# Performance work log

Hardware: AMD Instinct MI355X
Metric: run time of the kernel (lower is better)

The kernel has to match this reference:

```python
import jax, jax.numpy as jnp
import numpy as np

N_NODES = 100000


def sage_conv(x, src, dst, w_self, w_nei, b):
    # mean aggregation over incoming edges (src -> dst)
    agg = jax.ops.segment_sum(x[src], dst, num_segments=N_NODES)          # [N, d]
    deg = jax.ops.segment_sum(jnp.ones((src.shape[0], 1), x.dtype), dst,
                              num_segments=N_NODES)                        # [N, 1]
    mean = agg / jnp.maximum(deg, 1.0)
    return x @ w_self + mean @ w_nei + b


def setup_inputs() -> dict:
    key = jax.random.key(0)
    ks = jax.random.split(key, 12)
    d_in, d_hid, d_out = 64, 64, 64
    E = 1600000
    s = lambda d: 1.0 / np.sqrt(d)
    return {
        "x": jax.random.normal(ks[0], (N_NODES, d_in), jnp.float32),
        "edge_index": jax.random.randint(ks[1], (2, E), 0, N_NODES, jnp.int64),
        "w_self1": jax.random.normal(ks[2], (d_in, d_hid), jnp.float32) * s(d_in),
        "w_nei1": jax.random.normal(ks[3], (d_in, d_hid), jnp.float32) * s(d_in),
        "b1": jnp.zeros((d_hid,), jnp.float32),
        "w_self2": jax.random.normal(ks[4], (d_hid, d_hid), jnp.float32) * s(d_hid),
        "w_nei2": jax.random.normal(ks[5], (d_hid, d_hid), jnp.float32) * s(d_hid),
        "b2": jnp.zeros((d_hid,), jnp.float32),
        "w_self3": jax.random.normal(ks[6], (d_hid, d_out), jnp.float32) * s(d_hid),
        "w_nei3": jax.random.normal(ks[7], (d_hid, d_out), jnp.float32) * s(d_hid),
        "b3": jnp.zeros((d_out,), jnp.float32),
    }


def reference(x, edge_index, w_self1, w_nei1, b1, w_self2, w_nei2, b2,
              w_self3, w_nei3, b3):
    src, dst = edge_index[0], edge_index[1]
    h = jax.nn.relu(sage_conv(x, src, dst, w_self1, w_nei1, b1))
    h = jax.nn.relu(sage_conv(h, src, dst, w_self2, w_nei2, b2))
    h = sage_conv(h, src, dst, w_self3, w_nei3, b3)
    return h
```

## Files before the change

### kernel.cpp

```cpp
#include <hip/hip_runtime.h>
#include <hip/hip_bf16.h>

#define PB   512

typedef short bf16x8 __attribute__((ext_vector_type(8)));
typedef float f32x4  __attribute__((ext_vector_type(4)));

__device__ __forceinline__ unsigned short f2bf(float f) {
    unsigned u = __float_as_uint(f);
    u += 0x7FFFu + ((u >> 16) & 1u);
    return (unsigned short)(u >> 16);
}


__global__ __launch_bounds__(256) void part_hist(const int* __restrict__ dst,
                                                 int* __restrict__ counts,
                                                 int E, int NB) {
    __shared__ int h[512];
    const int tid = threadIdx.x;
    for (int i = tid; i < NB; i += 256) h[i] = 0;
    __syncthreads();
    const int per = (E + PB - 1) / PB;
    const int s = blockIdx.x * per;
    const int e = min(E, s + per);
    for (int i = s + tid; i < e; i += 256) atomicAdd(&h[dst[i] >> 8], 1);
    __syncthreads();
    for (int i = tid; i < NB; i += 256) counts[i * PB + blockIdx.x] = h[i];
}

__global__ __launch_bounds__(256) void scanA(const int* __restrict__ in,
                                             int* __restrict__ excl,
                                             int* __restrict__ bsums, int M) {
    __shared__ int tmp[256];
    const int tid = threadIdx.x;
    const int g = blockIdx.x * 256 + tid;
    int v = (g < M) ? in[g] : 0;
    tmp[tid] = v;
    __syncthreads();
    for (int off = 1; off < 256; off <<= 1) {
        int t = (tid >= off) ? tmp[tid - off] : 0;
        __syncthreads();
        tmp[tid] += t;
        __syncthreads();
    }
    if (g < M) excl[g] = tmp[tid] - v;
    if (tid == 255) bsums[blockIdx.x] = tmp[255];
}

__global__ __launch_bounds__(1024) void scanB(int* bsums, int nb) {
    __shared__ int tmp[1024];
    const int tid = threadIdx.x;
    int v = (tid < nb) ? bsums[tid] : 0;
    tmp[tid] = v;
    __syncthreads();
    for (int off = 1; off < 1024; off <<= 1) {
        int t = (tid >= off) ? tmp[tid - off] : 0;
        __syncthreads();
        tmp[tid] += t;
        __syncthreads();
    }
    if (tid < nb) bsums[tid] = tmp[tid] - v;
}

__global__ __launch_bounds__(256) void scanC(int* __restrict__ seg_base,
                                             const int* __restrict__ bsums,
                                             int* __restrict__ bucket_base,
                                             int M, int NB, int E) {
    const int g = blockIdx.x * 256 + threadIdx.x;
    if (g < M) {
        const int v = seg_base[g] + bsums[g >> 8];
        seg_base[g] = v;
        if ((g & (PB - 1)) == 0) bucket_base[g / PB] = v;
    }
    if (g == 0) bucket_base[NB] = E;
}

__global__ __launch_bounds__(256) void part_scatter(const int* __restrict__ src,
                                                    const int* __restrict__ dst,
                                                    const int* __restrict__ seg_base,
                                                    int* __restrict__ pairs,
                                                    int E, int NB) {
    __shared__ int cur[512];
    const int tid = threadIdx.x;
    for (int i = tid; i < NB; i += 256) cur[i] = seg_base[i * PB + blockIdx.x];
    __syncthreads();
    const int per = (E + PB - 1) / PB;
    const int s = blockIdx.x * per;
    const int e = min(E, s + per);
    for (int i = s + tid; i < e; i += 256) {
        const int d = dst[i];
        const int b = d >> 8;
        const int slot = atomicAdd(&cur[b], 1);
        pairs[slot] = src[i] | ((d & 255) << 20);
    }
}

__global__ __launch_bounds__(256) void csr_finalize(const int* __restrict__ pairs,
                                                    const int* __restrict__ bucket_base,
                                                    int* __restrict__ row_start,
                                                    int* __restrict__ col,
                                                    int N, int E) {
    __shared__ int h[256];
    __shared__ int tmp[256];
    __shared__ int cur[256];
    const int tid = threadIdx.x;
    const int b = blockIdx.x;
    const int node0 = b << 8;
    const int pbeg = bucket_base[b];
    const int pend = bucket_base[b + 1];
    h[tid] = 0;
    __syncthreads();
    for (int i = pbeg + tid; i < pend; i += 256)
        atomicAdd(&h[(pairs[i] >> 20) & 255], 1);
    __syncthreads();
    const int v = h[tid];
    tmp[tid] = v;
    __syncthreads();
    for (int off = 1; off < 256; off <<= 1) {
        int t = (tid >= off) ? tmp[tid - off] : 0;
        __syncthreads();
        tmp[tid] += t;
        __syncthreads();
    }
    const int excl = tmp[tid] - v;
    cur[tid] = pbeg + excl;
    if (node0 + tid < N) row_start[node0 + tid] = pbeg + excl;
    if (b == 0 && tid == 0) row_start[N] = E;
    __syncthreads();
    for (int i = pbeg + tid; i < pend; i += 256) {
        const int p = pairs[i];
        const int slot = atomicAdd(&cur[(p >> 20) & 255], 1);
        col[slot] = p & 0xFFFFF;
    }
}

__global__ __launch_bounds__(256) void to_bf16_kernel(const float* __restrict__ in,
                                                      unsigned short* __restrict__ out,
                                                      int n8) {
    const int g = blockIdx.x * 256 + threadIdx.x;
    if (g >= n8) return;
    const float4 v0 = *(const float4*)(in + (size_t)g * 8);
    const float4 v1 = *(const float4*)(in + (size_t)g * 8 + 4);
    uint4 o;
    o.x = (unsigned)f2bf(v0.x) | ((unsigned)f2bf(v0.y) << 16);
    o.y = (unsigned)f2bf(v0.z) | ((unsigned)f2bf(v0.w) << 16);
    o.z = (unsigned)f2bf(v1.x) | ((unsigned)f2bf(v1.y) << 16);
    o.w = (unsigned)f2bf(v1.z) | ((unsigned)f2bf(v1.w) << 16);
    *(uint4*)(out + (size_t)g * 8) = o;
}

__global__ __launch_bounds__(256) void pack_w_kernel(const float* __restrict__ Ws,
                                                     const float* __restrict__ Wn,
                                                     unsigned short* __restrict__ bswp) {
    const int i = blockIdx.x * 256 + threadIdx.x;
    if (i >= 8192) return;
    const int j = i & 7;
    const int L = (i >> 3) & 63;
    const int t = (i >> 9) & 3;
    const int s = i >> 11;
    const int k = s * 32 + ((L >> 4) << 3) + j;
    const int n = t * 16 + (L & 15);
    const float v = (k < 64) ? Ws[k * 64 + n] : Wn[(k - 64) * 64 + n];
    bswp[i] = f2bf(v);
}

#define ACC8(A, V)                                                    \
    A##0 += __uint_as_float((V).x << 16);                             \
    A##1 += __uint_as_float((V).x & 0xFFFF0000u);                     \
    A##2 += __uint_as_float((V).y << 16);                             \
    A##3 += __uint_as_float((V).y & 0xFFFF0000u);                     \
    A##4 += __uint_as_float((V).z << 16);                             \
    A##5 += __uint_as_float((V).z & 0xFFFF0000u);                     \
    A##6 += __uint_as_float((V).w << 16);                             \
    A##7 += __uint_as_float((V).w & 0xFFFF0000u);

__global__ __launch_bounds__(256) void gather_mean_kernel(
        const unsigned short* __restrict__ xb, const int* __restrict__ col,
        const int* __restrict__ row_start, unsigned short* __restrict__ meanb, int N) {
    const int tid = threadIdx.x;
    const int node = blockIdx.x * 32 + (tid >> 3);
    const int c8 = (tid & 7) * 8;
    if (node >= N) return;
    const int beg = row_start[node];
    const int end = row_start[node + 1];

    float a0 = 0.f, a1 = 0.f, a2 = 0.f, a3 = 0.f, a4 = 0.f, a5 = 0.f, a6 = 0.f, a7 = 0.f;
    float b0 = 0.f, b1 = 0.f, b2 = 0.f, b3 = 0.f, b4 = 0.f, b5 = 0.f, b6 = 0.f, b7 = 0.f;

    int i = beg;
    for (; i + 4 <= end; i += 4) {
        const int s0 = col[i + 0];
        const int s1 = col[i + 1];
        const int s2 = col[i + 2];
        const int s3 = col[i + 3];
        const uint4 v0 = *(const uint4*)(xb + (size_t)s0 * 64 + c8);
        const uint4 v1 = *(const uint4*)(xb + (size_t)s1 * 64 + c8);
        const uint4 v2 = *(const uint4*)(xb + (size_t)s2 * 64 + c8);
        const uint4 v3 = *(const uint4*)(xb + (size_t)s3 * 64 + c8);
        ACC8(a, v0)
        ACC8(b, v1)
        ACC8(a, v2)
        ACC8(b, v3)
    }
    for (; i < end; ++i) {
        const int s = col[i];
        const uint4 v = *(const uint4*)(xb + (size_t)s * 64 + c8);
        ACC8(a, v)
    }

    const float rd = 1.0f / fmaxf((float)(end - beg), 1.0f);
    const float m0 = (a0 + b0) * rd, m1 = (a1 + b1) * rd;
    const float m2 = (a2 + b2) * rd, m3 = (a3 + b3) * rd;
    const float m4 = (a4 + b4) * rd, m5 = (a5 + b5) * rd;
    const float m6 = (a6 + b6) * rd, m7 = (a7 + b7) * rd;
    uint4 o;
    o.x = (unsigned)f2bf(m0) | ((unsigned)f2bf(m1) << 16);
    o.y = (unsigned)f2bf(m2) | ((unsigned)f2bf(m3) << 16);
    o.z = (unsigned)f2bf(m4) | ((unsigned)f2bf(m5) << 16);
    o.w = (unsigned)f2bf(m6) | ((unsigned)f2bf(m7) << 16);
    *(uint4*)(meanb + (size_t)node * 64 + c8) = o;
}

__global__ __launch_bounds__(256) void mfma_update_kernel(
        const unsigned short* __restrict__ xb,
        const unsigned short* __restrict__ meanb,
        const unsigned short* __restrict__ bswp,
        const float* __restrict__ bias,
        float* __restrict__ outf,
        unsigned short* __restrict__ outb,
        int N, int do_relu) {
    const int tid  = threadIdx.x;
    const int lane = tid & 63;
    const int wave = tid >> 6;
    const int m    = lane & 15;
    const int quad = lane >> 4;
    const int node0 = blockIdx.x * 64 + wave * 16;

    int arow = node0 + m;
    if (arow >= N) arow = N - 1;
    const unsigned short* xr = xb    + (size_t)arow * 64 + quad * 8;
    const unsigned short* mr = meanb + (size_t)arow * 64 + quad * 8;

    f32x4 acc[4];
#pragma unroll
    for (int t = 0; t < 4; ++t) {
        const float b = bias[t * 16 + m];
        acc[t] = (f32x4){b, b, b, b};
    }

#pragma unroll
    for (int s = 0; s < 4; ++s) {
        bf16x8 a;
        if (s < 2) a = *(const bf16x8*)(xr + s * 32);
        else       a = *(const bf16x8*)(mr + (s - 2) * 32);
#pragma unroll
        for (int t = 0; t < 4; ++t) {
            const bf16x8 bf = *(const bf16x8*)(bswp + (((s * 4 + t) * 64 + lane) << 3));
            acc[t] = __builtin_amdgcn_mfma_f32_16x16x32_bf16(a, bf, acc[t], 0, 0, 0);
        }
    }

#pragma unroll
    for (int t = 0; t < 4; ++t) {
        const int colg = t * 16 + m;
#pragma unroll
        for (int r = 0; r < 4; ++r) {
            const int node = node0 + quad * 4 + r;
            if (node < N) {
                float v = acc[t][r];
                if (do_relu) v = fmaxf(v, 0.f);
                if (outf) outf[(size_t)node * 64 + colg] = v;
                if (outb) outb[(size_t)node * 64 + colg] = f2bf(v);
            }
        }
    }
}

extern "C" void kernel_launch(void* const* d_in, const int* in_sizes, int n_in,
                              void* d_out, int out_size, void* d_ws, size_t ws_size,
                              hipStream_t stream) {
    const float* x   = (const float*)d_in[0];
    const int*   ei  = (const int*)d_in[1];
    const float* ws1 = (const float*)d_in[2];
    const float* wn1 = (const float*)d_in[3];
    const float* b1  = (const float*)d_in[4];
    const float* ws2 = (const float*)d_in[5];
    const float* wn2 = (const float*)d_in[6];
    const float* b2  = (const float*)d_in[7];
    const float* ws3 = (const float*)d_in[8];
    const float* wn3 = (const float*)d_in[9];
    const float* b3  = (const float*)d_in[10];

    const int N = in_sizes[0] / 64;
    const int E = in_sizes[1] / 2;
    const int* src = ei;
    const int* dst = ei + E;
    const int NB = (N + 255) >> 8;
    const int M  = NB * PB;

    float* out = (float*)d_out;

    auto align256 = [](size_t v) { return (v + 255) / 256 * 256; };
    char* p = (char*)d_ws;
    int* counts      = (int*)p; p += align256((size_t)M * 4);
    int* seg_base    = (int*)p; p += align256((size_t)M * 4);
    int* bsums       = (int*)p; p += align256(1024 * 4);
    int* bucket_base = (int*)p; p += align256((size_t)(NB + 1) * 4);
    int* row_start   = (int*)p; p += align256((size_t)(N + 1) * 4);
    int* pairs       = (int*)p; p += align256((size_t)E * 4);
    int* col         = (int*)p; p += align256((size_t)E * 4);
    unsigned short* xb    = (unsigned short*)p; p += align256((size_t)N * 64 * 2);
    unsigned short* meanb = (unsigned short*)p; p += align256((size_t)N * 64 * 2);
    unsigned short* bw1   = (unsigned short*)p; p += align256(8192 * 2);
    unsigned short* bw2   = (unsigned short*)p; p += align256(8192 * 2);
    unsigned short* bw3   = (unsigned short*)p; p += align256(8192 * 2);

    const int scan_blocks = (M + 255) / 256;
    const int gm_blocks   = (N + 31) / 32;
    const int upd_blocks  = (N + 63) / 64;
    const int cvt_blocks  = (N * 64 / 8 + 255) / 256;

    part_hist   <<<PB, 256, 0, stream>>>(dst, counts, E, NB);
    scanA       <<<scan_blocks, 256, 0, stream>>>(counts, seg_base, bsums, M);
    scanB       <<<1, 1024, 0, stream>>>(bsums, scan_blocks);
    scanC       <<<scan_blocks, 256, 0, stream>>>(seg_base, bsums, bucket_base, M, NB, E);
    part_scatter<<<PB, 256, 0, stream>>>(src, dst, seg_base, pairs, E, NB);
    csr_finalize<<<NB, 256, 0, stream>>>(pairs, bucket_base, row_start, col, N, E);

    pack_w_kernel<<<32, 256, 0, stream>>>(ws1, wn1, bw1);
    pack_w_kernel<<<32, 256, 0, stream>>>(ws2, wn2, bw2);
    pack_w_kernel<<<32, 256, 0, stream>>>(ws3, wn3, bw3);
    to_bf16_kernel<<<cvt_blocks, 256, 0, stream>>>(x, xb, N * 64 / 8);

    gather_mean_kernel<<<gm_blocks, 256, 0, stream>>>(xb, col, row_start, meanb, N);
    mfma_update_kernel<<<upd_blocks, 256, 0, stream>>>(xb, meanb, bw1, b1, nullptr, xb, N, 1);
    gather_mean_kernel<<<gm_blocks, 256, 0, stream>>>(xb, col, row_start, meanb, N);
    mfma_update_kernel<<<upd_blocks, 256, 0, stream>>>(xb, meanb, bw2, b2, nullptr, xb, N, 1);
    gather_mean_kernel<<<gm_blocks, 256, 0, stream>>>(xb, col, row_start, meanb, N);
    mfma_update_kernel<<<upd_blocks, 256, 0, stream>>>(xb, meanb, bw3, b3, out, nullptr, N, 0);
}
```

Baseline: 276.4 us.

## Fuse neighbor mean gather with MFMA update per layer and batch weight packing

Merges the gather-mean and MFMA linear update into one kernel per layer. Each block computes the bf16 means for its 64 nodes into shared memory and then feeds them straight to the MFMA. This removes the global round trip of the mean buffer and three kernel launches. Ping-pong feature buffers replace the in-place update, since other blocks may still be gathering the old features. The three weight-pack launches are merged into one. The cost is that each block now spends longer in the irregular gather before its MFMA phase.

```diff
diff --git a/kernel.cpp b/kernel.cpp
--- a/kernel.cpp
+++ b/kernel.cpp
@@ -149,19 +149,25 @@
     *(uint4*)(out + (size_t)g * 8) = o;
 }
 
-__global__ __launch_bounds__(256) void pack_w_kernel(const float* __restrict__ Ws,
-                                                     const float* __restrict__ Wn,
-                                                     unsigned short* __restrict__ bswp) {
+__global__ __launch_bounds__(256) void pack_w3_kernel(
+        const float* __restrict__ Ws1, const float* __restrict__ Wn1,
+        const float* __restrict__ Ws2, const float* __restrict__ Wn2,
+        const float* __restrict__ Ws3, const float* __restrict__ Wn3,
+        unsigned short* __restrict__ bw) {
     const int i = blockIdx.x * 256 + threadIdx.x;
-    if (i >= 8192) return;
-    const int j = i & 7;
-    const int L = (i >> 3) & 63;
-    const int t = (i >> 9) & 3;
-    const int s = i >> 11;
+    if (i >= 3 * 8192) return;
+    const int w = i >> 13;
+    const int r = i & 8191;
+    const float* Ws = (w == 0) ? Ws1 : (w == 1) ? Ws2 : Ws3;
+    const float* Wn = (w == 0) ? Wn1 : (w == 1) ? Wn2 : Wn3;
+    const int j = r & 7;
+    const int L = (r >> 3) & 63;
+    const int t = (r >> 9) & 3;
+    const int s = r >> 11;
     const int k = s * 32 + ((L >> 4) << 3) + j;
     const int n = t * 16 + (L & 15);
     const float v = (k < 64) ? Ws[k * 64 + n] : Wn[(k - 64) * 64 + n];
-    bswp[i] = f2bf(v);
+    bw[i] = f2bf(v);
 }
 
 #define ACC8(A, V)                                                    \
@@ -174,72 +180,72 @@
     A##6 += __uint_as_float((V).w << 16);                             \
     A##7 += __uint_as_float((V).w & 0xFFFF0000u);
 
-__global__ __launch_bounds__(256) void gather_mean_kernel(
-        const unsigned short* __restrict__ xb, const int* __restrict__ col,
-        const int* __restrict__ row_start, unsigned short* __restrict__ meanb, int N) {
-    const int tid = threadIdx.x;
-    const int node = blockIdx.x * 32 + (tid >> 3);
-    const int c8 = (tid & 7) * 8;
-    if (node >= N) return;
-    const int beg = row_start[node];
-    const int end = row_start[node + 1];
-
-    float a0 = 0.f, a1 = 0.f, a2 = 0.f, a3 = 0.f, a4 = 0.f, a5 = 0.f, a6 = 0.f, a7 = 0.f;
-    float b0 = 0.f, b1 = 0.f, b2 = 0.f, b3 = 0.f, b4 = 0.f, b5 = 0.f, b6 = 0.f, b7 = 0.f;
-
-    int i = beg;
-    for (; i + 4 <= end; i += 4) {
-        const int s0 = col[i + 0];
-        const int s1 = col[i + 1];
-        const int s2 = col[i + 2];
-        const int s3 = col[i + 3];
-        const uint4 v0 = *(const uint4*)(xb + (size_t)s0 * 64 + c8);
-        const uint4 v1 = *(const uint4*)(xb + (size_t)s1 * 64 + c8);
-        const uint4 v2 = *(const uint4*)(xb + (size_t)s2 * 64 + c8);
-        const uint4 v3 = *(const uint4*)(xb + (size_t)s3 * 64 + c8);
-        ACC8(a, v0)
-        ACC8(b, v1)
-        ACC8(a, v2)
-        ACC8(b, v3)
-    }
-    for (; i < end; ++i) {
-        const int s = col[i];
-        const uint4 v = *(const uint4*)(xb + (size_t)s * 64 + c8);
-        ACC8(a, v)
-    }
-
-    const float rd = 1.0f / fmaxf((float)(end - beg), 1.0f);
-    const float m0 = (a0 + b0) * rd, m1 = (a1 + b1) * rd;
-    const float m2 = (a2 + b2) * rd, m3 = (a3 + b3) * rd;
-    const float m4 = (a4 + b4) * rd, m5 = (a5 + b5) * rd;
-    const float m6 = (a6 + b6) * rd, m7 = (a7 + b7) * rd;
-    uint4 o;
-    o.x = (unsigned)f2bf(m0) | ((unsigned)f2bf(m1) << 16);
-    o.y = (unsigned)f2bf(m2) | ((unsigned)f2bf(m3) << 16);
-    o.z = (unsigned)f2bf(m4) | ((unsigned)f2bf(m5) << 16);
-    o.w = (unsigned)f2bf(m6) | ((unsigned)f2bf(m7) << 16);
-    *(uint4*)(meanb + (size_t)node * 64 + c8) = o;
-}
-
-__global__ __launch_bounds__(256) void mfma_update_kernel(
-        const unsigned short* __restrict__ xb,
-        const unsigned short* __restrict__ meanb,
-        const unsigned short* __restrict__ bswp,
-        const float* __restrict__ bias,
+__global__ __launch_bounds__(256) void sage_fused_kernel(
+        const unsigned short* __restrict__ xin, const int* __restrict__ col,
+        const int* __restrict__ row_start,
+        const unsigned short* __restrict__ bswp, const float* __restrict__ bias,
+        unsigned short* __restrict__ outb,
         float* __restrict__ outf,
-        unsigned short* __restrict__ outb,
         int N, int do_relu) {
-    const int tid  = threadIdx.x;
+    __shared__ __align__(16) unsigned short smean[64][72];
+
+    const int tid = threadIdx.x;
+    const int node0 = blockIdx.x * 64;
+
+    for (int r = 0; r < 2; ++r) {
+        const int nl = r * 32 + (tid >> 3);
+        const int node = node0 + nl;
+        const int c8 = (tid & 7) * 8;
+        float a0 = 0.f, a1 = 0.f, a2 = 0.f, a3 = 0.f, a4 = 0.f, a5 = 0.f, a6 = 0.f, a7 = 0.f;
+        float b0 = 0.f, b1 = 0.f, b2 = 0.f, b3 = 0.f, b4 = 0.f, b5 = 0.f, b6 = 0.f, b7 = 0.f;
+        float rd = 0.f;
+        if (node < N) {
+            const int beg = row_start[node];
+            const int end = row_start[node + 1];
+            int i = beg;
+            for (; i + 4 <= end; i += 4) {
+                const int s0 = col[i + 0];
+                const int s1 = col[i + 1];
+                const int s2 = col[i + 2];
+                const int s3 = col[i + 3];
+                const uint4 v0 = *(const uint4*)(xin + (size_t)s0 * 64 + c8);
+                const uint4 v1 = *(const uint4*)(xin + (size_t)s1 * 64 + c8);
+                const uint4 v2 = *(const uint4*)(xin + (size_t)s2 * 64 + c8);
+                const uint4 v3 = *(const uint4*)(xin + (size_t)s3 * 64 + c8);
+                ACC8(a, v0)
+                ACC8(b, v1)
+                ACC8(a, v2)
+                ACC8(b, v3)
+            }
+            for (; i < end; ++i) {
+                const int s = col[i];
+                const uint4 v = *(const uint4*)(xin + (size_t)s * 64 + c8);
+                ACC8(a, v)
+            }
+            rd = 1.0f / fmaxf((float)(end - beg), 1.0f);
+        }
+        const float m0 = (a0 + b0) * rd, m1 = (a1 + b1) * rd;
+        const float m2 = (a2 + b2) * rd, m3 = (a3 + b3) * rd;
+        const float m4 = (a4 + b4) * rd, m5 = (a5 + b5) * rd;
+        const float m6 = (a6 + b6) * rd, m7 = (a7 + b7) * rd;
+        uint4 o;
+        o.x = (unsigned)f2bf(m0) | ((unsigned)f2bf(m1) << 16);
+        o.y = (unsigned)f2bf(m2) | ((unsigned)f2bf(m3) << 16);
+        o.z = (unsigned)f2bf(m4) | ((unsigned)f2bf(m5) << 16);
+        o.w = (unsigned)f2bf(m6) | ((unsigned)f2bf(m7) << 16);
+        *(uint4*)(&smean[nl][c8]) = o;
+    }
+    __syncthreads();
+
     const int lane = tid & 63;
     const int wave = tid >> 6;
     const int m    = lane & 15;
     const int quad = lane >> 4;
-    const int node0 = blockIdx.x * 64 + wave * 16;
-
-    int arow = node0 + m;
+    const int nw0  = node0 + wave * 16;
+
+    int arow = nw0 + m;
     if (arow >= N) arow = N - 1;
-    const unsigned short* xr = xb    + (size_t)arow * 64 + quad * 8;
-    const unsigned short* mr = meanb + (size_t)arow * 64 + quad * 8;
+    const unsigned short* xr = xin + (size_t)arow * 64 + quad * 8;
 
     f32x4 acc[4];
 #pragma unroll
@@ -252,7 +258,7 @@
     for (int s = 0; s < 4; ++s) {
         bf16x8 a;
         if (s < 2) a = *(const bf16x8*)(xr + s * 32);
-        else       a = *(const bf16x8*)(mr + (s - 2) * 32);
+        else       a = *(const bf16x8*)(&smean[wave * 16 + m][(s - 2) * 32 + quad * 8]);
 #pragma unroll
         for (int t = 0; t < 4; ++t) {
             const bf16x8 bf = *(const bf16x8*)(bswp + (((s * 4 + t) * 64 + lane) << 3));
@@ -265,7 +271,7 @@
         const int colg = t * 16 + m;
 #pragma unroll
         for (int r = 0; r < 4; ++r) {
-            const int node = node0 + quad * 4 + r;
+            const int node = nw0 + quad * 4 + r;
             if (node < N) {
                 float v = acc[t][r];
                 if (do_relu) v = fmaxf(v, 0.f);
@@ -309,15 +315,12 @@
     int* row_start   = (int*)p; p += align256((size_t)(N + 1) * 4);
     int* pairs       = (int*)p; p += align256((size_t)E * 4);
     int* col         = (int*)p; p += align256((size_t)E * 4);
-    unsigned short* xb    = (unsigned short*)p; p += align256((size_t)N * 64 * 2);
-    unsigned short* meanb = (unsigned short*)p; p += align256((size_t)N * 64 * 2);
-    unsigned short* bw1   = (unsigned short*)p; p += align256(8192 * 2);
-    unsigned short* bw2   = (unsigned short*)p; p += align256(8192 * 2);
-    unsigned short* bw3   = (unsigned short*)p; p += align256(8192 * 2);
+    unsigned short* xb  = (unsigned short*)p; p += align256((size_t)N * 64 * 2);
+    unsigned short* xb2 = (unsigned short*)p; p += align256((size_t)N * 64 * 2);
+    unsigned short* bw  = (unsigned short*)p; p += align256(3 * 8192 * 2);
 
     const int scan_blocks = (M + 255) / 256;
-    const int gm_blocks   = (N + 31) / 32;
-    const int upd_blocks  = (N + 63) / 64;
+    const int fused_blocks = (N + 63) / 64;
     const int cvt_blocks  = (N * 64 / 8 + 255) / 256;
 
     part_hist   <<<PB, 256, 0, stream>>>(dst, counts, E, NB);
@@ -327,15 +330,10 @@
     part_scatter<<<PB, 256, 0, stream>>>(src, dst, seg_base, pairs, E, NB);
     csr_finalize<<<NB, 256, 0, stream>>>(pairs, bucket_base, row_start, col, N, E);
 
-    pack_w_kernel<<<32, 256, 0, stream>>>(ws1, wn1, bw1);
-    pack_w_kernel<<<32, 256, 0, stream>>>(ws2, wn2, bw2);
-    pack_w_kernel<<<32, 256, 0, stream>>>(ws3, wn3, bw3);
+    pack_w3_kernel<<<96, 256, 0, stream>>>(ws1, wn1, ws2, wn2, ws3, wn3, bw);
     to_bf16_kernel<<<cvt_blocks, 256, 0, stream>>>(x, xb, N * 64 / 8);
 
-    gather_mean_kernel<<<gm_blocks, 256, 0, stream>>>(xb, col, row_start, meanb, N);
-    mfma_update_kernel<<<upd_blocks, 256, 0, stream>>>(xb, meanb, bw1, b1, nullptr, xb, N, 1);
-    gather_mean_kernel<<<gm_blocks, 256, 0, stream>>>(xb, col, row_start, meanb, N);
-    mfma_update_kernel<<<upd_blocks, 256, 0, stream>>>(xb, meanb, bw2, b2, nullptr, xb, N, 1);
-    gather_mean_kernel<<<gm_blocks, 256, 0, stream>>>(xb, col, row_start, meanb, N);
-    mfma_update_kernel<<<upd_blocks, 256, 0, stream>>>(xb, meanb, bw3, b3, out, nullptr, N, 0);
-}
+    sage_fused_kernel<<<fused_blocks, 256, 0, stream>>>(xb,  col, row_start, bw,          b1, xb2,     nullptr, N, 1);
+    sage_fused_kernel<<<fused_blocks, 256, 0, stream>>>(xb2, col, row_start, bw + 8192,   b2, xb,      nullptr, N, 1);
+    sage_fused_kernel<<<fused_blocks, 256, 0, stream>>>(xb,  col, row_start, bw + 16384,  b3, nullptr, out,     N, 0);
+}
```

Measured after the change: 272.5 us. About the same (-1.4%).
